# Kernel optimization log

Hardware: AMD Instinct MI355X
Metric: run time of the kernel (lower is better)

## Reference

```python
import jax, jax.numpy as jnp
import numpy as np

NEG_SLOPE = 0.2  # PyG GATv2Conv default negative_slope


def _gatv2_layer(x, src, dst, Wl, Wr, att, bias, heads, out_ch, concat, num_nodes):
    # x: [N, F_in]; src/dst: [E'] (self-loops already appended)
    N, H, C = num_nodes, heads, out_ch
    xl = (x @ Wl).reshape(N, H, C)  # source-side transform (lin_l)
    xr = (x @ Wr).reshape(N, H, C)  # target-side transform (lin_r)
    m = xl[src] + xr[dst]                       # [E', H, C]
    e = jax.nn.leaky_relu(m, NEG_SLOPE)
    logits = jnp.einsum('ehc,hc->eh', e, att)   # [E', H]
    # numerically stable segment softmax over incoming edges of each dst node
    mx = jax.ops.segment_max(logits, dst, num_segments=N)   # [N, H]
    ex = jnp.exp(logits - mx[dst])
    den = jax.ops.segment_sum(ex, dst, num_segments=N)      # [N, H]
    alpha = ex / den[dst]                                    # [E', H]
    out = jax.ops.segment_sum(alpha[:, :, None] * xl[src], dst, num_segments=N)  # [N, H, C]
    out = out.reshape(N, H * C) if concat else out.mean(axis=1)
    return out + bias


def setup_inputs() -> dict:
    key = jax.random.key(0)
    N, E = 50000, 800000
    IN, HID, OUT, HEADS = 128, 32, 64, 4
    ks = jax.random.split(key, 16)
    x = jax.random.normal(ks[0], (N, IN), dtype=jnp.float32)
    edge_index = jax.random.randint(ks[1], (2, E), 0, N, dtype=jnp.int64)

    def lin(k, fin, fout):
        return jax.random.normal(k, (fin, fout), dtype=jnp.float32) * (1.0 / np.sqrt(fin))

    HC = HID * HEADS  # 128
    inp = {
        'x': x, 'edge_index': edge_index,
        # layer 1: IN -> HID x HEADS, concat
        'Wl1': lin(ks[2], IN, HC), 'Wr1': lin(ks[3], IN, HC),
        'a1': jax.random.normal(ks[4], (HEADS, HID), dtype=jnp.float32) * 0.1,
        'b1': jnp.zeros((HC,), dtype=jnp.float32),
        # layer 2: HC -> HID x HEADS, concat
        'Wl2': lin(ks[5], HC, HC), 'Wr2': lin(ks[6], HC, HC),
        'a2': jax.random.normal(ks[7], (HEADS, HID), dtype=jnp.float32) * 0.1,
        'b2': jnp.zeros((HC,), dtype=jnp.float32),
        # layer 3: HC -> OUT, heads=1, concat=False
        'Wl3': lin(ks[8], HC, OUT), 'Wr3': lin(ks[9], HC, OUT),
        'a3': jax.random.normal(ks[10], (1, OUT), dtype=jnp.float32) * 0.1,
        'b3': jnp.zeros((OUT,), dtype=jnp.float32),
    }
    return inp


def reference(x, edge_index, Wl1, Wr1, a1, b1, Wl2, Wr2, a2, b2, Wl3, Wr3, a3, b3):
    N = x.shape[0]
    # PyG GATv2Conv default add_self_loops=True
    loops = jnp.arange(N, dtype=edge_index.dtype)
    src = jnp.concatenate([edge_index[0], loops])
    dst = jnp.concatenate([edge_index[1], loops])
    HID, HEADS, OUT = 32, 4, 64
    h = _gatv2_layer(x, src, dst, Wl1, Wr1, a1, b1, HEADS, HID, True, N)
    h = jax.nn.elu(h)  # eval mode: dropout is identity
    h = _gatv2_layer(h, src, dst, Wl2, Wr2, a2, b2, HEADS, HID, True, N)
    h = jax.nn.elu(h)
    out = _gatv2_layer(h, src, dst, Wl3, Wr3, a3, b3, 1, OUT, False, N)
    return out
```

## Files before the change

kernel.cpp:

```cpp
#include <hip/hip_runtime.h>
#include <cstdint>
#include <cstddef>
#include <math.h>

#define NEG_SLOPE 0.2f
#define DEGB 512
#define EB 4096

typedef unsigned short ushort_t;
typedef __attribute__((ext_vector_type(8))) short short8;
typedef __attribute__((ext_vector_type(4))) float f32x4;
typedef _Float16 half8 __attribute__((ext_vector_type(8)));
typedef _Float16 half2_t __attribute__((ext_vector_type(2)));

__device__ __forceinline__ ushort_t f2bf(float f) {
    unsigned u = __float_as_uint(f);
    unsigned r = u + 0x7FFFu + ((u >> 16) & 1u);
    return (ushort_t)(r >> 16);
}
__device__ __forceinline__ float bf2f(ushort_t h) {
    return __uint_as_float(((unsigned)h) << 16);
}
__device__ __forceinline__ ushort_t f2h(float f) {
    _Float16 h = (_Float16)f;
    return *(ushort_t*)&h;
}

__device__ __forceinline__ float dot2acc(half2_t a, half2_t b, float c) {
#if __has_builtin(__builtin_amdgcn_fdot2)
    return __builtin_amdgcn_fdot2(a, b, c, false);
#else
    return c + (float)a[0] * (float)b[0] + (float)a[1] * (float)b[1];
#endif
}

template<int CTRL>
__device__ __forceinline__ float dpp_add(float p) {
    int t = __builtin_amdgcn_update_dpp(0, __builtin_bit_cast(int, p),
                                        CTRL, 0xF, 0xF, true);
    return p + __builtin_bit_cast(float, t);
}

__device__ __forceinline__ float swz4_add(float p) {
    int t = __builtin_amdgcn_ds_swizzle(__builtin_bit_cast(int, p), 0x101F);
    return p + __builtin_bit_cast(float, t);
}

__device__ __forceinline__ int wave_incl_scan(int v, int lane) {
    #pragma unroll
    for (int o = 1; o < 64; o <<= 1) {
        int t = __shfl_up(v, o, 64);
        if (lane >= o) v += t;
    }
    return v;
}


__global__ void colscan(int* __restrict__ blkcnt, int nblk, int* __restrict__ btot,
                        int* __restrict__ dhist) {
    int b = blockIdx.x;
    int lane = threadIdx.x;
    if (lane < 2) dhist[b * 2 + lane] = 0;
    int running = 0;
    for (int base = 0; base < nblk; base += 64) {
        int idx = base + lane;
        int v = (idx < nblk) ? blkcnt[idx * 256 + b] : 0;
        int incl = wave_incl_scan(v, lane);
        if (idx < nblk) blkcnt[idx * 256 + b] = running + incl - v;
        running += __shfl(incl, 63, 64);
    }
    if (lane == 0) btot[b] = running;
}

__global__ void bucketscan(const int* __restrict__ btot, int* __restrict__ bbase) {
    __shared__ int tmp[256];
    int t = threadIdx.x;
    int v = btot[t];
    tmp[t] = v;
    __syncthreads();
    for (int o = 1; o < 256; o <<= 1) {
        int x = (t >= o) ? tmp[t - o] : 0;
        __syncthreads();
        tmp[t] += x;
        __syncthreads();
    }
    bbase[t] = tmp[t] - v;
}

__global__ void bucket_scatter(const int* __restrict__ ei, int E, int Et,
                               const int* __restrict__ blkrel,
                               const int* __restrict__ bbase,
                               unsigned* __restrict__ ebuf) {
    __shared__ int base_l[256];
    __shared__ int cnt[256];
    int t = threadIdx.x;
    base_l[t] = bbase[t] + blkrel[blockIdx.x * 256 + t];
    cnt[t] = 0;
    __syncthreads();
    int e0 = blockIdx.x * EB;
    #pragma unroll
    for (int it = 0; it < EB / 256; ++it) {
        int e = e0 + it * 256 + t;
        if (e < Et) {
            int s, d;
            if (e < E) { s = ei[e]; d = ei[E + e]; }
            else       { s = d = e - E; }
            int b = d >> 8;
            int r = atomicAdd(&cnt[b], 1);
            ebuf[base_l[b] + r] = (unsigned)s | (((unsigned)d & 255u) << 17);
        }
    }
}

__global__ void bucket_deg_scan_hist(const unsigned* __restrict__ ebuf,
                                     const int* __restrict__ bbase,
                                     const int* __restrict__ btot,
                                     int N, int* __restrict__ deg,
                                     int* __restrict__ rowstart,
                                     int* __restrict__ partials,
                                     int* __restrict__ dhist) {
    __shared__ int dcnt[256];
    __shared__ int tmp[256];
    __shared__ int h[DEGB];
    int b = blockIdx.x, t = threadIdx.x;
    dcnt[t] = 0;
    h[t] = 0; h[t + 256] = 0;
    __syncthreads();
    int s0 = bbase[b], c = btot[b];
    for (int i = t; i < c; i += 256)
        atomicAdd(&dcnt[ebuf[s0 + i] >> 17], 1);
    __syncthreads();
    int node = b * 256 + t;
    int dv = dcnt[t];
    if (node < N) deg[node] = dv;
    tmp[t] = dv;
    __syncthreads();
    for (int o = 1; o < 256; o <<= 1) {
        int x = (t >= o) ? tmp[t - o] : 0;
        __syncthreads();
        tmp[t] += x;
        __syncthreads();
    }
    if (node < N) rowstart[node] = tmp[t] - dv;
    if (t == 255) partials[b] = tmp[255];
    if (node < N) {
        int dc = dv < DEGB - 1 ? dv : DEGB - 1;
        atomicAdd(&h[dc], 1);
    }
    __syncthreads();
    int c0 = h[t];       if (c0) atomicAdd(&dhist[t], c0);
    int c1 = h[t + 256]; if (c1) atomicAdd(&dhist[t + 256], c1);
}

__global__ void finalize_scans(int* __restrict__ rowstart,
                               const int* __restrict__ partials, int nbkt, int N,
                               const int* __restrict__ dhist,
                               int* __restrict__ dstart) {
    __shared__ int tmp[DEGB];
    int t = threadIdx.x;
    int b = blockIdx.x;
    if (b < nbkt) {
        if (t < 256) tmp[t] = (t < nbkt) ? partials[t] : 0;
        __syncthreads();
        for (int o = 1; o < 256; o <<= 1) {
            int x = (t < 256 && t >= o) ? tmp[t - o] : 0;
            __syncthreads();
            if (t < 256) tmp[t] += x;
            __syncthreads();
        }
        int off = (b > 0) ? tmp[b - 1] : 0;
        int node = b * 256 + t;
        if (t < 256 && node < N) rowstart[node] += off;
    } else {
        int v = dhist[t];
        tmp[t] = v;
        __syncthreads();
        for (int o = 1; o < DEGB; o <<= 1) {
            int x = (t >= o) ? tmp[t - o] : 0;
            __syncthreads();
            tmp[t] += x;
            __syncthreads();
        }
        dstart[t] = tmp[DEGB - 1] - tmp[t];
    }
}

__global__ void csr_perm_scatter(const unsigned* __restrict__ ebuf,
                                 const int* __restrict__ bbase,
                                 const int* __restrict__ btot,
                                 const int* __restrict__ rowstart,
                                 const int* __restrict__ deg, int N,
                                 int* __restrict__ dstart,
                                 int* __restrict__ csr_src,
                                 int4* __restrict__ desc) {
    __shared__ int cur[256];
    __shared__ int h[DEGB];
    __shared__ int base[DEGB];
    int b = blockIdx.x, t = threadIdx.x;
    int node = b * 256 + t;
    int rs = (node < N) ? rowstart[node] : 0;
    cur[t] = rs;
    h[t] = 0; h[t + 256] = 0;
    __syncthreads();
    int s0 = bbase[b], c = btot[b];
    for (int i = t; i < c; i += 256) {
        unsigned v = ebuf[s0 + i];
        int pos = atomicAdd(&cur[v >> 17], 1);
        csr_src[pos] = (int)(v & 0x1FFFFu);
    }
    int dv = (node < N) ? deg[node] : 0;
    int dc = dv < DEGB - 1 ? dv : DEGB - 1;
    int r = 0;
    if (node < N) r = atomicAdd(&h[dc], 1);
    __syncthreads();
    int c0 = h[t];       if (c0) base[t]       = atomicAdd(&dstart[t], c0);
    int c1 = h[t + 256]; if (c1) base[t + 256] = atomicAdd(&dstart[t + 256], c1);
    __syncthreads();
    if (node < N) desc[base[dc] + r] = make_int4(node, rs, dv, 0);
}

template<int MOUT, bool CONVA>
__global__ __launch_bounds__(256) void gemm_mfma(const ushort_t* __restrict__ Ah,
                                                 const ushort_t* __restrict__ Al,
                                                 const float* __restrict__ Af,
                                                 const float* __restrict__ Wl,
                                                 const float* __restrict__ Wr,
                                                 ushort_t* __restrict__ xlh,
                                                 ushort_t* __restrict__ xrh, int N,
                                                 const int* __restrict__ ei,
                                                 int E, int Et,
                                                 int* __restrict__ blkcnt,
                                                 int histBlocks) {
    constexpr int NT  = MOUT / 16;
    constexpr int FPT = MOUT / 8;
    constexpr int CPR = MOUT / 4;
    __shared__ __align__(16) ushort_t Bh[NT * 2048];
    __shared__ __align__(16) ushort_t Bl[NT * 2048];
    const int tid = threadIdx.x;

    if ((int)blockIdx.x < histBlocks) {
        int* cnt = (int*)Bh;
        cnt[tid] = 0;
        __syncthreads();
        int e0 = blockIdx.x * EB;
        #pragma unroll
        for (int it = 0; it < EB / 256; ++it) {
            int e = e0 + it * 256 + tid;
            if (e < Et) {
                int d = (e < E) ? ei[E + e] : (e - E);
                atomicAdd(&cnt[d >> 8], 1);
            }
        }
        __syncthreads();
        blkcnt[blockIdx.x * 256 + tid] = cnt[tid];
        return;
    }

    const int g     = (int)blockIdx.x - histBlocks;
    const int row0  = (g >> 1) * 128;
    const bool isR  = (g & 1) != 0;
    const float* W  = isR ? Wr : Wl;
    ushort_t* OUT   = isR ? xrh : xlh;

    #pragma unroll
    for (int i = 0; i < FPT; ++i) {
        int idx = tid * FPT + i;
        int k   = idx / CPR;
        int c4  = (idx % CPR) * 4;
        float4 w = *(const float4*)(W + (size_t)k * MOUT + c4);
        float wv[4] = {w.x, w.y, w.z, w.w};
        int q = k >> 5, quad = (k >> 3) & 3, j = k & 7;
        #pragma unroll
        for (int e = 0; e < 4; ++e) {
            int c = c4 + e;
            int t = c >> 4;
            int l = (quad << 4) | (c & 15);
            int pos = ((t * 4 + q) * 64 + l) * 8 + j;
            ushort_t hb = f2bf(wv[e]);
            Bh[pos] = hb;
            Bl[pos] = f2bf(wv[e] - bf2f(hb));
        }
    }
    __syncthreads();

    const int wv_  = tid >> 6;
    const int lane = tid & 63;
    const int m    = lane & 15;
    const int quad = lane >> 4;
    const int wrow0 = row0 + wv_ * 32;

    f32x4 acc[2][NT] = {};

    for (int q = 0; q < 4; ++q) {
        short8 ahf[2], alf[2];
        #pragma unroll
        for (int r = 0; r < 2; ++r) {
            int row = wrow0 + 16 * r + m;
            row = row < N ? row : N - 1;
            size_t off = (size_t)row * 128 + q * 32 + quad * 8;
            if constexpr (CONVA) {
                float4 f0 = *(const float4*)(Af + off);
                float4 f1 = *(const float4*)(Af + off + 4);
                float fv[8] = {f0.x, f0.y, f0.z, f0.w, f1.x, f1.y, f1.z, f1.w};
                short ah[8], al[8];
                #pragma unroll
                for (int e = 0; e < 8; ++e) {
                    ushort_t hb = f2bf(fv[e]);
                    ah[e] = (short)hb;
                    al[e] = (short)f2bf(fv[e] - bf2f(hb));
                }
                ahf[r] = short8{ah[0],ah[1],ah[2],ah[3],ah[4],ah[5],ah[6],ah[7]};
                alf[r] = short8{al[0],al[1],al[2],al[3],al[4],al[5],al[6],al[7]};
            } else {
                ahf[r] = *(const short8*)(Ah + off);
                alf[r] = *(const short8*)(Al + off);
            }
        }
        #pragma unroll
        for (int t = 0; t < NT; ++t) {
            int base = ((t * 4 + q) * 64 + lane) * 8;
            short8 bh = *(const short8*)(Bh + base);
            short8 bl = *(const short8*)(Bl + base);
            #pragma unroll
            for (int r = 0; r < 2; ++r) {
                acc[r][t] = __builtin_amdgcn_mfma_f32_16x16x32_bf16(ahf[r], bh, acc[r][t], 0, 0, 0);
                acc[r][t] = __builtin_amdgcn_mfma_f32_16x16x32_bf16(ahf[r], bl, acc[r][t], 0, 0, 0);
                acc[r][t] = __builtin_amdgcn_mfma_f32_16x16x32_bf16(alf[r], bh, acc[r][t], 0, 0, 0);
            }
        }
    }

    #pragma unroll
    for (int r = 0; r < 2; ++r)
        #pragma unroll
        for (int i = 0; i < 4; ++i) {
            int row = wrow0 + 16 * r + quad * 4 + i;
            if (row < N) {
                #pragma unroll
                for (int t = 0; t < NT; ++t)
                    OUT[(size_t)row * MOUT + t * 16 + m] = f2h(acc[r][t][i]);
            }
        }
}

template<int H, int C, bool ELU, int OMODE>
__global__ __launch_bounds__(512) void node_attn(const ushort_t* __restrict__ xlh,
                                                 const ushort_t* __restrict__ xrh,
                                                 const float* __restrict__ att,
                                                 const float* __restrict__ bias,
                                                 const int4* __restrict__ desc,
                                                 const int* __restrict__ csr_src,
                                                 int N, float* __restrict__ out,
                                                 ushort_t* __restrict__ outh,
                                                 ushort_t* __restrict__ outl) {
    constexpr int HC  = H * C;
    constexpr int VPT = 8;
    constexpr int LPG = HC / VPT;
    constexpr int GPW = 64 / LPG;
    constexpr int GROUP = C / VPT;
    constexpr int DR  = 5;

    const int lane = threadIdx.x & 63;
    const int wv   = threadIdx.x >> 6;
    const int gid  = lane / LPG;
    const int lig  = lane % LPG;
    const int ch0  = lig * VPT;

    const int s = (blockIdx.x * 8 + wv) * GPW + gid;
    if (s >= N) return;

    half2_t a2[4];
    {
        float4 u0 = *(const float4*)(att + ch0);
        float4 u1 = *(const float4*)(att + ch0 + 4);
        a2[0] = half2_t{(_Float16)u0.x, (_Float16)u0.y};
        a2[1] = half2_t{(_Float16)u0.z, (_Float16)u0.w};
        a2[2] = half2_t{(_Float16)u1.x, (_Float16)u1.y};
        a2[3] = half2_t{(_Float16)u1.z, (_Float16)u1.w};
    }
    float bias8[VPT];
    {
        float4 b0 = *(const float4*)(bias + ch0);
        float4 b1 = *(const float4*)(bias + ch0 + 4);
        bias8[0]=b0.x; bias8[1]=b0.y; bias8[2]=b0.z; bias8[3]=b0.w;
        bias8[4]=b1.x; bias8[5]=b1.y; bias8[6]=b1.z; bias8[7]=b1.w;
    }
    const half2_t c02 = half2_t{(_Float16)NEG_SLOPE, (_Float16)NEG_SLOPE};

    const int4 dsc = desc[s];
    const int n  = dsc.x;
    const int j0 = dsc.y;
    const int dg = dsc.z;

    half8 xrv = *(const half8*)(xrh + (size_t)n * HC + ch0);

    auto ldidx = [&](int e) {
        int ee = e < dg ? e : dg - 1;
        return csr_src[j0 + ee];
    };
    auto ldrow = [&](int idx) -> half8 {
        return *(const half8*)(xlh + (size_t)(unsigned)idx * HC + ch0);
    };

    float d = 0.f;
    float acc[VPT] = {};

    auto process = [&](half8 v) {
        float p = 0.f;
        #pragma unroll
        for (int i = 0; i < 4; ++i) {
            half2_t v2 = half2_t{v[2 * i], v[2 * i + 1]};
            half2_t x2 = half2_t{xrv[2 * i], xrv[2 * i + 1]};
            half2_t m2 = v2 + x2;
            half2_t lr = __builtin_elementwise_max(m2, c02 * m2);
            p = dot2acc(lr, a2[i], p);
        }
        if constexpr (GROUP >= 2) p = dpp_add<0xB1>(p);
        if constexpr (GROUP >= 4) p = dpp_add<0x4E>(p);
        if constexpr (GROUP >= 8) p = swz4_add(p);
        float pe = __expf(p);
        d += pe;
        #pragma unroll
        for (int i = 0; i < VPT; ++i)
            acc[i] += pe * (float)v[i];
    };

    int   ibuf[DR];
    half8 rbuf[DR];
    #pragma unroll
    for (int k = 0; k < DR; ++k) ibuf[k] = ldidx(k);
    #pragma unroll
    for (int k = 0; k < DR; ++k) {
        rbuf[k] = ldrow(ibuf[k]);
        ibuf[k] = ldidx(k + DR);
    }

    int e = 0;
    for (; e + DR <= dg; e += DR) {
        #pragma unroll
        for (int k = 0; k < DR; ++k) {
            half8 v = rbuf[k];
            rbuf[k] = ldrow(ibuf[k]);
            ibuf[k] = ldidx(e + k + 2 * DR);
            process(v);
        }
    }
    #pragma unroll
    for (int k = 0; k < DR; ++k)
        if (e + k < dg) process(rbuf[k]);

    float inv = 1.f / d;
    float vv[VPT];
    #pragma unroll
    for (int i = 0; i < VPT; ++i) {
        float v = acc[i] * inv + bias8[i];
        if (ELU) v = v > 0.f ? v : (__expf(v) - 1.f);
        vv[i] = v;
    }
    if (OMODE == 0) {
        *(float4*)(out + (size_t)n * HC + ch0) =
            make_float4(vv[0], vv[1], vv[2], vv[3]);
        *(float4*)(out + (size_t)n * HC + ch0 + 4) =
            make_float4(vv[4], vv[5], vv[6], vv[7]);
    } else {
        ushort_t hb[VPT], lb[VPT];
        #pragma unroll
        for (int i = 0; i < VPT; ++i) {
            hb[i] = f2bf(vv[i]);
            lb[i] = f2bf(vv[i] - bf2f(hb[i]));
        }
        *(ushort4*)(outh + (size_t)n * HC + ch0) =
            ushort4{hb[0], hb[1], hb[2], hb[3]};
        *(ushort4*)(outh + (size_t)n * HC + ch0 + 4) =
            ushort4{hb[4], hb[5], hb[6], hb[7]};
        *(ushort4*)(outl + (size_t)n * HC + ch0) =
            ushort4{lb[0], lb[1], lb[2], lb[3]};
        *(ushort4*)(outl + (size_t)n * HC + ch0 + 4) =
            ushort4{lb[4], lb[5], lb[6], lb[7]};
    }
}

extern "C" void kernel_launch(void* const* d_in, const int* in_sizes, int n_in,
                              void* d_out, int out_size, void* d_ws, size_t ws_size,
                              hipStream_t stream) {
    const float* x   = (const float*)d_in[0];
    const int*   ei  = (const int*)d_in[1];
    const float* Wl1 = (const float*)d_in[2];
    const float* Wr1 = (const float*)d_in[3];
    const float* a1  = (const float*)d_in[4];
    const float* b1  = (const float*)d_in[5];
    const float* Wl2 = (const float*)d_in[6];
    const float* Wr2 = (const float*)d_in[7];
    const float* a2  = (const float*)d_in[8];
    const float* b2  = (const float*)d_in[9];
    const float* Wl3 = (const float*)d_in[10];
    const float* Wr3 = (const float*)d_in[11];
    const float* a3  = (const float*)d_in[12];
    const float* b3  = (const float*)d_in[13];

    const int N  = in_sizes[0] / 128;
    const int E  = in_sizes[1] / 2;
    const int Et = E + N;
    const int nb = (N + 255) / 256;

    char* p = (char*)d_ws;
    auto alloc = [&](size_t bytes) -> void* {
        void* r = (void*)p;
        p += (bytes + 255) & ~(size_t)255;
        return r;
    };
    const int ebBlocks = (Et + EB - 1) / EB;
    int*      csr_src  = (int*)alloc((size_t)Et * 4 + 256);
    unsigned* ebuf     = (unsigned*)alloc((size_t)Et * 4);
    int*      blkcnt   = (int*)alloc((size_t)ebBlocks * 256 * 4);
    int*      btot     = (int*)alloc(256 * 4);
    int*      bbase    = (int*)alloc(256 * 4);
    int*      deg      = (int*)alloc((size_t)N * 4);
    int*      rowstart = (int*)alloc((size_t)N * 4);
    int*      partials = (int*)alloc((size_t)nb * 4);
    int4*     desc     = (int4*)alloc((size_t)N * 16);
    int*      dhist    = (int*)alloc((size_t)DEGB * 4);
    int*      dstart   = (int*)alloc((size_t)DEGB * 4);
    ushort_t* xlh      = (ushort_t*)alloc((size_t)N * 128 * 2);
    ushort_t* xrh      = (ushort_t*)alloc((size_t)N * 128 * 2);
    ushort_t* Ah       = (ushort_t*)alloc((size_t)N * 128 * 2);
    ushort_t* Al       = (ushort_t*)alloc((size_t)N * 128 * 2);

    const int rowBlocks    = (N + 127) / 128;
    const int nodeBlocks12 = (N + 31) / 32;
    const int nodeBlocks3  = (N + 63) / 64;

    gemm_mfma<128, true><<<ebBlocks + rowBlocks * 2, 256, 0, stream>>>(
        nullptr, nullptr, x, Wl1, Wr1, xlh, xrh, N, ei, E, Et, blkcnt, ebBlocks);

    colscan<<<256, 64, 0, stream>>>(blkcnt, ebBlocks, btot, dhist);
    bucketscan<<<1, 256, 0, stream>>>(btot, bbase);
    bucket_scatter<<<ebBlocks, 256, 0, stream>>>(ei, E, Et, blkcnt, bbase, ebuf);
    bucket_deg_scan_hist<<<nb, 256, 0, stream>>>(ebuf, bbase, btot, N,
                                                 deg, rowstart, partials, dhist);
    finalize_scans<<<nb + 1, DEGB, 0, stream>>>(rowstart, partials, nb, N,
                                                dhist, dstart);
    csr_perm_scatter<<<nb, 256, 0, stream>>>(ebuf, bbase, btot, rowstart, deg, N,
                                             dstart, csr_src, desc);

    node_attn<4, 32, true, 1><<<nodeBlocks12, 512, 0, stream>>>(
        xlh, xrh, a1, b1, desc, csr_src, N, nullptr, Ah, Al);

    gemm_mfma<128, false><<<rowBlocks * 2, 256, 0, stream>>>(
        Ah, Al, nullptr, Wl2, Wr2, xlh, xrh, N, nullptr, 0, 0, nullptr, 0);
    node_attn<4, 32, true, 1><<<nodeBlocks12, 512, 0, stream>>>(
        xlh, xrh, a2, b2, desc, csr_src, N, nullptr, Ah, Al);

    float* out = (float*)d_out;
    gemm_mfma<64, false><<<rowBlocks * 2, 256, 0, stream>>>(
        Ah, Al, nullptr, Wl3, Wr3, xlh, xrh, N, nullptr, 0, 0, nullptr, 0);
    node_attn<1, 64, false, 0><<<nodeBlocks3, 512, 0, stream>>>(
        xlh, xrh, a3, b3, desc, csr_src, N, out, nullptr, nullptr);
}
```

Before: 280.5 us.

## Fold bucket and finalize scans into consumer kernels to cut launches

Removes the single-block bucketscan and the finalize_scans kernels. Each consumer block now recomputes the prefix sums it needs (bucket base, row offset, degree-histogram start) redundantly in shared memory, and a separate dcur counter array replaces dstart. This drops two kernel launches and their serialization gaps from the CSR build, in exchange for extra per-block reduction work and extra barriers.

```diff
diff --git a/kernel.cpp b/kernel.cpp
--- a/kernel.cpp
+++ b/kernel.cpp
@@ -57,10 +57,10 @@
 
 
 __global__ void colscan(int* __restrict__ blkcnt, int nblk, int* __restrict__ btot,
-                        int* __restrict__ dhist) {
+                        int* __restrict__ dhist, int* __restrict__ dcur) {
     int b = blockIdx.x;
     int lane = threadIdx.x;
-    if (lane < 2) dhist[b * 2 + lane] = 0;
+    if (lane < 2) { dhist[b * 2 + lane] = 0; dcur[b * 2 + lane] = 0; }
     int running = 0;
     for (int base = 0; base < nblk; base += 64) {
         int idx = base + lane;
@@ -72,11 +72,17 @@
     if (lane == 0) btot[b] = running;
 }
 
-__global__ void bucketscan(const int* __restrict__ btot, int* __restrict__ bbase) {
+__global__ void bucket_scatter(const int* __restrict__ ei, int E, int Et,
+                               const int* __restrict__ blkrel,
+                               const int* __restrict__ btot,
+                               unsigned* __restrict__ ebuf) {
+    __shared__ int base_l[256];
     __shared__ int tmp[256];
+    __shared__ int cnt[256];
     int t = threadIdx.x;
     int v = btot[t];
     tmp[t] = v;
+    cnt[t] = 0;
     __syncthreads();
     for (int o = 1; o < 256; o <<= 1) {
         int x = (t >= o) ? tmp[t - o] : 0;
@@ -84,18 +90,7 @@
         tmp[t] += x;
         __syncthreads();
     }
-    bbase[t] = tmp[t] - v;
-}
-
-__global__ void bucket_scatter(const int* __restrict__ ei, int E, int Et,
-                               const int* __restrict__ blkrel,
-                               const int* __restrict__ bbase,
-                               unsigned* __restrict__ ebuf) {
-    __shared__ int base_l[256];
-    __shared__ int cnt[256];
-    int t = threadIdx.x;
-    base_l[t] = bbase[t] + blkrel[blockIdx.x * 256 + t];
-    cnt[t] = 0;
+    base_l[t] = (tmp[t] - v) + blkrel[blockIdx.x * 256 + t];
     __syncthreads();
     int e0 = blockIdx.x * EB;
     #pragma unroll
@@ -113,7 +108,6 @@
 }
 
 __global__ void bucket_deg_scan_hist(const unsigned* __restrict__ ebuf,
-                                     const int* __restrict__ bbase,
                                      const int* __restrict__ btot,
                                      int N, int* __restrict__ deg,
                                      int* __restrict__ rowstart,
@@ -125,8 +119,16 @@
     int b = blockIdx.x, t = threadIdx.x;
     dcnt[t] = 0;
     h[t] = 0; h[t + 256] = 0;
-    __syncthreads();
-    int s0 = bbase[b], c = btot[b];
+    tmp[t] = (t < b) ? btot[t] : 0;
+    __syncthreads();
+    #pragma unroll
+    for (int o = 128; o > 0; o >>= 1) {
+        if (t < o) tmp[t] += tmp[t + o];
+        __syncthreads();
+    }
+    const int s0 = tmp[0];
+    const int c  = btot[b];
+    __syncthreads();
     for (int i = t; i < c; i += 256)
         atomicAdd(&dcnt[ebuf[s0 + i] >> 17], 1);
     __syncthreads();
@@ -152,57 +154,63 @@
     int c1 = h[t + 256]; if (c1) atomicAdd(&dhist[t + 256], c1);
 }
 
-__global__ void finalize_scans(int* __restrict__ rowstart,
-                               const int* __restrict__ partials, int nbkt, int N,
-                               const int* __restrict__ dhist,
-                               int* __restrict__ dstart) {
-    __shared__ int tmp[DEGB];
-    int t = threadIdx.x;
-    int b = blockIdx.x;
-    if (b < nbkt) {
-        if (t < 256) tmp[t] = (t < nbkt) ? partials[t] : 0;
-        __syncthreads();
-        for (int o = 1; o < 256; o <<= 1) {
-            int x = (t < 256 && t >= o) ? tmp[t - o] : 0;
-            __syncthreads();
-            if (t < 256) tmp[t] += x;
-            __syncthreads();
-        }
-        int off = (b > 0) ? tmp[b - 1] : 0;
-        int node = b * 256 + t;
-        if (t < 256 && node < N) rowstart[node] += off;
-    } else {
-        int v = dhist[t];
-        tmp[t] = v;
-        __syncthreads();
-        for (int o = 1; o < DEGB; o <<= 1) {
-            int x = (t >= o) ? tmp[t - o] : 0;
-            __syncthreads();
-            tmp[t] += x;
-            __syncthreads();
-        }
-        dstart[t] = tmp[DEGB - 1] - tmp[t];
-    }
-}
-
 __global__ void csr_perm_scatter(const unsigned* __restrict__ ebuf,
-                                 const int* __restrict__ bbase,
                                  const int* __restrict__ btot,
                                  const int* __restrict__ rowstart,
+                                 const int* __restrict__ partials,
                                  const int* __restrict__ deg, int N,
-                                 int* __restrict__ dstart,
+                                 const int* __restrict__ dhist,
+                                 int* __restrict__ dcur,
                                  int* __restrict__ csr_src,
                                  int4* __restrict__ desc) {
     __shared__ int cur[256];
+    __shared__ int tmp[256];
     __shared__ int h[DEGB];
     __shared__ int base[DEGB];
     int b = blockIdx.x, t = threadIdx.x;
+
+    tmp[t] = (t < b) ? btot[t] : 0;
+    __syncthreads();
+    #pragma unroll
+    for (int o = 128; o > 0; o >>= 1) {
+        if (t < o) tmp[t] += tmp[t + o];
+        __syncthreads();
+    }
+    const int s0 = tmp[0];
+    __syncthreads();
+
+    tmp[t] = (t < b) ? partials[t] : 0;
+    __syncthreads();
+    #pragma unroll
+    for (int o = 128; o > 0; o >>= 1) {
+        if (t < o) tmp[t] += tmp[t + o];
+        __syncthreads();
+    }
+    const int roff = tmp[0];
+    __syncthreads();
+
+    h[t]       = dhist[t];
+    h[t + 256] = dhist[t + 256];
+    __syncthreads();
+    for (int o = 1; o < DEGB; o <<= 1) {
+        int v0 = (t >= o) ? h[t - o] : 0;
+        int v1 = (t + 256 >= o) ? h[t + 256 - o] : 0;
+        __syncthreads();
+        h[t] += v0;
+        h[t + 256] += v1;
+        __syncthreads();
+    }
+    int total = h[DEGB - 1];
+    base[t]       = total - h[t];
+    base[t + 256] = total - h[t + 256];
+    __syncthreads();
+
+    h[t] = 0; h[t + 256] = 0;
     int node = b * 256 + t;
-    int rs = (node < N) ? rowstart[node] : 0;
+    int rs = (node < N) ? rowstart[node] + roff : 0;
     cur[t] = rs;
-    h[t] = 0; h[t + 256] = 0;
-    __syncthreads();
-    int s0 = bbase[b], c = btot[b];
+    __syncthreads();
+    const int c = btot[b];
     for (int i = t; i < c; i += 256) {
         unsigned v = ebuf[s0 + i];
         int pos = atomicAdd(&cur[v >> 17], 1);
@@ -213,8 +221,8 @@
     int r = 0;
     if (node < N) r = atomicAdd(&h[dc], 1);
     __syncthreads();
-    int c0 = h[t];       if (c0) base[t]       = atomicAdd(&dstart[t], c0);
-    int c1 = h[t + 256]; if (c1) base[t + 256] = atomicAdd(&dstart[t + 256], c1);
+    int c0 = h[t];       if (c0) base[t]       += atomicAdd(&dcur[t], c0);
+    int c1 = h[t + 256]; if (c1) base[t + 256] += atomicAdd(&dcur[t + 256], c1);
     __syncthreads();
     if (node < N) desc[base[dc] + r] = make_int4(node, rs, dv, 0);
 }
@@ -514,13 +522,12 @@
     unsigned* ebuf     = (unsigned*)alloc((size_t)Et * 4);
     int*      blkcnt   = (int*)alloc((size_t)ebBlocks * 256 * 4);
     int*      btot     = (int*)alloc(256 * 4);
-    int*      bbase    = (int*)alloc(256 * 4);
     int*      deg      = (int*)alloc((size_t)N * 4);
     int*      rowstart = (int*)alloc((size_t)N * 4);
     int*      partials = (int*)alloc((size_t)nb * 4);
     int4*     desc     = (int4*)alloc((size_t)N * 16);
     int*      dhist    = (int*)alloc((size_t)DEGB * 4);
-    int*      dstart   = (int*)alloc((size_t)DEGB * 4);
+    int*      dcur     = (int*)alloc((size_t)DEGB * 4);
     ushort_t* xlh      = (ushort_t*)alloc((size_t)N * 128 * 2);
     ushort_t* xrh      = (ushort_t*)alloc((size_t)N * 128 * 2);
     ushort_t* Ah       = (ushort_t*)alloc((size_t)N * 128 * 2);
@@ -533,15 +540,12 @@
     gemm_mfma<128, true><<<ebBlocks + rowBlocks * 2, 256, 0, stream>>>(
         nullptr, nullptr, x, Wl1, Wr1, xlh, xrh, N, ei, E, Et, blkcnt, ebBlocks);
 
-    colscan<<<256, 64, 0, stream>>>(blkcnt, ebBlocks, btot, dhist);
-    bucketscan<<<1, 256, 0, stream>>>(btot, bbase);
-    bucket_scatter<<<ebBlocks, 256, 0, stream>>>(ei, E, Et, blkcnt, bbase, ebuf);
-    bucket_deg_scan_hist<<<nb, 256, 0, stream>>>(ebuf, bbase, btot, N,
+    colscan<<<256, 64, 0, stream>>>(blkcnt, ebBlocks, btot, dhist, dcur);
+    bucket_scatter<<<ebBlocks, 256, 0, stream>>>(ei, E, Et, blkcnt, btot, ebuf);
+    bucket_deg_scan_hist<<<nb, 256, 0, stream>>>(ebuf, btot, N,
                                                  deg, rowstart, partials, dhist);
-    finalize_scans<<<nb + 1, DEGB, 0, stream>>>(rowstart, partials, nb, N,
-                                                dhist, dstart);
-    csr_perm_scatter<<<nb, 256, 0, stream>>>(ebuf, bbase, btot, rowstart, deg, N,
-                                             dstart, csr_src, desc);
+    csr_perm_scatter<<<nb, 256, 0, stream>>>(ebuf, btot, rowstart, partials,
+                                             deg, N, dhist, dcur, csr_src, desc);
 
     node_attn<4, 32, true, 1><<<nodeBlocks12, 512, 0, stream>>>(
         xlh, xrh, a1, b1, desc, csr_src, N, nullptr, Ah, Al);
```

Result: no change. 276.0 us (-1.6%).
